# Kernel optimization log

Measured on AMD Instinct MI355X. Metric: run time of the kernel, lower is better.

The kernel has to match this reference:

```python
import jax, jax.numpy as jnp
import numpy as np

N = 50000      # nodes
E = 800000     # edges (avg degree 16)
IN, HID, OUT = 256, 128, 64
K, ALPHA = 4, 0.0  # APPNPConv(k=4, alpha=0.0)


def setup_inputs() -> dict:
    key = jax.random.key(0)
    ks = jax.random.split(key, 5)
    features = jax.random.normal(ks[0], (N, IN), jnp.float32)
    src = jax.random.randint(ks[1], (E,), 0, N, jnp.int32)
    dst = jax.random.randint(ks[2], (E,), 0, N, jnp.int32)
    W1 = jax.random.normal(ks[3], (IN, HID), jnp.float32) / np.float32(np.sqrt(IN))
    b1 = jnp.zeros((HID,), jnp.float32)
    W3 = jax.random.normal(ks[4], (HID, OUT), jnp.float32) / np.float32(np.sqrt(HID))
    b3 = jnp.zeros((OUT,), jnp.float32)
    return dict(features=features, src=src, dst=dst, W1=W1, b1=b1, W3=W3, b3=b3)


def _sym_norms(src, dst, n):
    # D_out^{-1/2} for source side, D_in^{-1/2} for destination side (DGL norm='both')
    ones = jnp.ones((src.shape[0],), jnp.float32)
    deg_out = jax.ops.segment_sum(ones, src, num_segments=n)
    deg_in = jax.ops.segment_sum(ones, dst, num_segments=n)
    return jnp.clip(deg_out, 1.0) ** -0.5, jnp.clip(deg_in, 1.0) ** -0.5


def _prop(x, src, dst, norm_src, norm_dst):
    # x: [N, D]. Symmetric-normalized SpMM: D_in^{-1/2} A D_out^{-1/2} x
    msg = (x * norm_src[:, None])[src]                       # [E, D] gather
    agg = jax.ops.segment_sum(msg, dst, num_segments=x.shape[0])  # [N, D] scatter-add
    return agg * norm_dst[:, None]


def reference(features, src, dst, W1, b1, W3, b3):
    ns, nd = _sym_norms(src, dst, N)
    # GraphConv 1 (weight-first since in_dim > hidden_dim; math identical either way)
    h = _prop(features @ W1, src, dst, ns, nd) + b1
    # dropout is identity in eval mode (training=False)
    # APPNPConv: k=4 power-iteration steps with teleport alpha=0.0
    h0 = h
    for _ in range(K):
        h = (1.0 - ALPHA) * _prop(h, src, dst, ns, nd) + ALPHA * h0
    # GraphConv 3
    out = _prop(h @ W3, src, dst, ns, nd) + b3
    return out
```

## Files before the change

### kernel.cpp

```cpp
#include <hip/hip_runtime.h>
#include <math.h>

#define N_NODES 50000
#define N_EDGES 800000
#define DIN 256
#define DHID 128
#define DOUT 64
#define CSTRIDE 64
#define ZROW N_NODES
#define HBLOCKS 256
#define HCHUNK (N_EDGES / HBLOCKS)
#define HWORDS (N_NODES / 4)
#define SLICE ((size_t)(N_NODES + 1) * 16)
#define NGROUPS (N_NODES / 4)
#define P2BLOCKS 196

#define SB_SENT 3125
#define SB_HS (SB_SENT + HBLOCKS)
#define SB_HD (SB_HS + HBLOCKS)
#define SB_TOT (SB_HD + 66)

__global__ void k_setup(const int* __restrict__ src, const int* __restrict__ dst,
                        unsigned int* __restrict__ pS, unsigned int* __restrict__ pD,
                        unsigned int* __restrict__ csr32,
                        const float* __restrict__ W1, const float* __restrict__ b1,
                        const float* __restrict__ W3,
                        float* __restrict__ W13, float* __restrict__ bb,
                        float* __restrict__ Y0, float* __restrict__ Y1) {
    __shared__ unsigned int h[HWORDS];
    int bx = blockIdx.x, t = threadIdx.x;
    if (bx < SB_SENT) {
        unsigned int v = (unsigned int)ZROW | ((unsigned int)ZROW << 16);
        uint2 o; o.x = v; o.y = v;
        ((uint2*)csr32)[bx * 256 + t] = o;
        return;
    }
    if (bx < SB_HD) {
        const int* idx = (bx < SB_HS) ? src : dst;
        unsigned int* outp = (bx < SB_HS) ? pS : pD;
        int hb = bx - ((bx < SB_HS) ? SB_SENT : SB_HS);
        for (int w = t; w < HWORDS; w += 256) h[w] = 0u;
        __syncthreads();
        int base = hb * HCHUNK;
        for (int i = t; i < HCHUNK; i += 256) {
            int s = idx[base + i];
            atomicAdd(&h[s >> 2], 1u << ((s & 3) << 3));
        }
        __syncthreads();
        outp += (size_t)hb * HWORDS;
        for (int w = t; w < HWORDS; w += 256) outp[w] = h[w];
        return;
    }
    int vb = bx - SB_HD;
    if (vb == 65) {
        if (t < 64) {
            int qq = t >> 4, c2 = t & 15;
            Y0[(size_t)qq * SLICE + ((size_t)ZROW << 4) + c2] = 0.f;
            Y1[(size_t)qq * SLICE + ((size_t)ZROW << 4) + c2] = 0.f;
        }
        return;
    }
    if (vb == 64) {
        if (t < DOUT) {
            float s = 0.f;
            for (int k = 0; k < DHID; ++k) s += b1[k] * W3[k * DOUT + t];
            bb[t] = s;
        }
        return;
    }
    int idx2 = vb * 256 + t;
    int i = idx2 >> 6, j = idx2 & 63;
    float s = 0.f;
    for (int k = 0; k < DHID; ++k) s += W1[i * DHID + k] * W3[k * DOUT + j];
    W13[idx2] = s;
}

__global__ void k_hpre(const unsigned int* __restrict__ pS,
                       const unsigned int* __restrict__ pD,
                       unsigned int* __restrict__ prefix,
                       int* __restrict__ deg_in,
                       float* __restrict__ ns, float* __restrict__ nd,
                       float* __restrict__ cc, int* __restrict__ dparts) {
    __shared__ unsigned int sdw[64][4];
    __shared__ unsigned int sow[64][4];
    __shared__ int lh[65];
    int t = threadIdx.x;
    if (t < 65) lh[t] = 0;
    int col = t >> 2, sub = t & 3;
    int wid = blockIdx.x * 64 + col;
    bool act = wid < HWORDS;
    unsigned int ps = 0, pd = 0;
    if (act) {
        int b0 = sub << 6;
#pragma unroll 4
        for (int b = b0; b < b0 + 64; ++b) {
            ps += pS[(size_t)b * HWORDS + wid];
            pd += pD[(size_t)b * HWORDS + wid];
        }
    }
    sdw[col][sub] = pd;
    sow[col][sub] = ps;
    __syncthreads();
    if (act) {
        unsigned int base = 0;
        for (int k = 0; k < sub; ++k) base += sdw[col][k];
        int b0 = sub << 6;
        unsigned int run = base;
        for (int b = b0; b < b0 + 64; ++b) {
            unsigned int w = pD[(size_t)b * HWORDS + wid];
            prefix[(size_t)b * HWORDS + wid] = run;
            run += w;
        }
        if (sub == 0) {
            unsigned int totd = sdw[col][0] + sdw[col][1] + sdw[col][2] + sdw[col][3];
            unsigned int toto = sow[col][0] + sow[col][1] + sow[col][2] + sow[col][3];
            unsigned int di[4] = {totd & 0xffu, (totd >> 8) & 0xffu,
                                  (totd >> 16) & 0xffu, totd >> 24};
            unsigned int dov[4] = {toto & 0xffu, (toto >> 8) & 0xffu,
                                   (toto >> 16) & 0xffu, toto >> 24};
            int4 dd; dd.x = (int)di[0]; dd.y = (int)di[1]; dd.z = (int)di[2]; dd.w = (int)di[3];
            *(int4*)(deg_in + (wid << 2)) = dd;
            float4 vns, vnd, vcc;
            float* pns = &vns.x; float* pnd = &vnd.x; float* pcc = &vcc.x;
#pragma unroll
            for (int q = 0; q < 4; ++q) {
                int bin = (int)di[q]; if (bin > 64) bin = 64;
                atomicAdd(&lh[bin], 1);
                unsigned int a = dov[q] < 1u ? 1u : dov[q];
                unsigned int b = di[q] < 1u ? 1u : di[q];
                float fa = 1.0f / sqrtf((float)a);
                float fb = 1.0f / sqrtf((float)b);
                pns[q] = fa; pnd[q] = fb; pcc[q] = fa * fb;
            }
            *(float4*)(ns + (wid << 2)) = vns;
            *(float4*)(nd + (wid << 2)) = vnd;
            *(float4*)(cc + (wid << 2)) = vcc;
        }
    }
    __syncthreads();
    if (t < 65) dparts[blockIdx.x * 65 + t] = lh[t];
}

__global__ void k_dscan(const int* __restrict__ dparts, int* __restrict__ offs) {
    __shared__ int colsum[65], binbase[65];
    int t = threadIdx.x;
    if (t < 65) {
        int s = 0;
        for (int b = 0; b < P2BLOCKS; ++b) s += dparts[b * 65 + t];
        colsum[t] = s;
    }
    __syncthreads();
    if (t == 0) {
        int run = 0;
        for (int k = 64; k >= 0; --k) { binbase[k] = run; run += colsum[k]; }
    }
    __syncthreads();
    if (t < 65) {
        int run = binbase[t];
        for (int b = 0; b < P2BLOCKS; ++b) { offs[b * 65 + t] = run; run += dparts[b * 65 + t]; }
    }
}

__global__ void k_dscatter(const int* __restrict__ deg_in, const int* __restrict__ offs,
                           const float* __restrict__ cc, const float* __restrict__ ns,
                           const float* __restrict__ nd,
                           int* __restrict__ perm, int* __restrict__ inv,
                           int* __restrict__ degP, float* __restrict__ ccP,
                           float* __restrict__ nsP, float* __restrict__ ndP) {
    __shared__ int off[65];
    int t = threadIdx.x;
    if (t < 65) off[t] = offs[blockIdx.x * 65 + t];
    __syncthreads();
    int wid = blockIdx.x * 64 + t;
    if (t < 64 && wid < HWORDS) {
        int4 d4 = *(const int4*)(deg_in + (wid << 2));
        int dd[4] = {d4.x, d4.y, d4.z, d4.w};
#pragma unroll
        for (int k = 0; k < 4; ++k) {
            int node = (wid << 2) + k;
            int bin = dd[k] > 64 ? 64 : dd[k];
            int slot = atomicAdd(&off[bin], 1);
            perm[slot] = node; inv[node] = slot;
            degP[slot] = dd[k];
            ccP[slot] = cc[node]; nsP[slot] = ns[node]; ndP[slot] = nd[node];
        }
    }
}

__global__ void k_fill(const int* __restrict__ src, const int* __restrict__ dst,
                       const unsigned int* __restrict__ prefix,
                       const int* __restrict__ inv,
                       unsigned short* __restrict__ csr) {
    __shared__ unsigned int h[HWORDS];
    int t = threadIdx.x;
    const unsigned int* prow = prefix + (size_t)blockIdx.x * HWORDS;
    for (int w = t; w < HWORDS; w += 256) h[w] = prow[w];
    __syncthreads();
    int base = blockIdx.x * HCHUNK;
    for (int i = t; i < HCHUNK; i += 256) {
        int s = src[base + i], d = dst[base + i];
        int sh = (d & 3) << 3;
        unsigned int old = atomicAdd(&h[d >> 2], 1u << sh);
        int slot = (int)((old >> sh) & 0xffu);
        csr[((size_t)inv[d] << 6) + slot] = (unsigned short)inv[s];
    }
}

__global__ void k_gemm(const float* __restrict__ X, const float* __restrict__ W13,
                       const float* __restrict__ ns, const int* __restrict__ inv,
                       float* __restrict__ Y) {
    __shared__ float As[16][68];
    __shared__ float Bs[16][64];
    int tid = threadIdx.x;
    int tx = tid & 15, ty = tid >> 4;
    int row0 = blockIdx.x * 64;
    float acc[4][4];
#pragma unroll
    for (int i = 0; i < 4; ++i)
#pragma unroll
        for (int j = 0; j < 4; ++j) acc[i][j] = 0.f;

    int lr = tid >> 2;
    int lk = (tid & 3) << 2;
    int arow = row0 + lr;
    if (arow > N_NODES - 1) arow = N_NODES - 1;

    for (int k0 = 0; k0 < DIN; k0 += 16) {
        float4 a = *(const float4*)(X + (size_t)arow * DIN + k0 + lk);
        As[lk + 0][lr] = a.x; As[lk + 1][lr] = a.y;
        As[lk + 2][lr] = a.z; As[lk + 3][lr] = a.w;
        float4 b = *(const float4*)(W13 + (size_t)(k0 + (tid >> 4)) * DOUT + ((tid & 15) << 2));
        *(float4*)&Bs[tid >> 4][(tid & 15) << 2] = b;
        __syncthreads();
#pragma unroll
        for (int k = 0; k < 16; ++k) {
            float4 av = *(const float4*)&As[k][ty << 2];
            float4 bv = *(const float4*)&Bs[k][tx << 2];
            float ar[4] = {av.x, av.y, av.z, av.w};
            float br[4] = {bv.x, bv.y, bv.z, bv.w};
#pragma unroll
            for (int i = 0; i < 4; ++i)
#pragma unroll
                for (int j = 0; j < 4; ++j) acc[i][j] += ar[i] * br[j];
        }
        __syncthreads();
    }
    int qq = tx >> 2;
    int co = (tx & 3) << 2;
#pragma unroll
    for (int i = 0; i < 4; ++i) {
        int row = row0 + (ty << 2) + i;
        if (row < N_NODES) {
            float nsr = ns[row];
            int prow = inv[row];
            float4 o;
            o.x = acc[i][0] * nsr; o.y = acc[i][1] * nsr;
            o.z = acc[i][2] * nsr; o.w = acc[i][3] * nsr;
            *(float4*)(Y + (size_t)qq * SLICE + ((size_t)prow << 4) + co) = o;
        }
    }
}


template <int MODE>
__launch_bounds__(256, 8)
__global__ void k_spmm(const float* __restrict__ xs, float* __restrict__ ys,
                       const unsigned short* __restrict__ csr,
                       const int* __restrict__ degP,
                       const float* __restrict__ ccP, const float* __restrict__ nsP,
                       const float* __restrict__ ndP,
                       const float* __restrict__ bb, const float* __restrict__ b3,
                       const int* __restrict__ perm) {
    __shared__ unsigned short rows[4][256];
    int wid  = threadIdx.x >> 6;
    int lane = threadIdx.x & 63;
    int q    = (blockIdx.x & 7) >> 1;
    int half = blockIdx.x & 1;
    int g    = (blockIdx.x >> 3) * 8 + wid * 2 + half;
    if (g >= NGROUPS) return;
    int node0 = g << 2;

    int nn = lane >> 4, sl = lane & 15;
    const uint2* crow = (const uint2*)(csr + ((size_t)(node0 + nn) << 6)) + sl;
    uint2 rv = *crow;
    unsigned short* bp = &rows[wid][(sl << 4) + nn];
    bp[0]  = (unsigned short)(rv.x & 0xffffu);
    bp[4]  = (unsigned short)(rv.x >> 16);
    bp[8]  = (unsigned short)(rv.y & 0xffffu);
    bp[12] = (unsigned short)(rv.y >> 16);

    int n0u = __builtin_amdgcn_readfirstlane(node0);
    int m = (degP[n0u] + 7) & ~7;

    int n = lane >> 4, e = (lane >> 2) & 3, c4 = lane & 3;
    const unsigned short* rd = &rows[wid][(e << 2) + n];
    const float* xq = xs + (size_t)q * SLICE + (c4 << 2);

    float ax = 0.f, ay = 0.f, az = 0.f, aw = 0.f;
#define LDV(T) const float4 v##T = *(const float4*)(xq + ((size_t)rd[16 * (T)] << 4))
#define ACCV(T) ax += v##T.x; ay += v##T.y; az += v##T.z; aw += v##T.w
    if (m <= 8) {
        LDV(0); LDV(1);
        ACCV(0); ACCV(1);
    } else if (m <= 16) {
        LDV(0); LDV(1); LDV(2); LDV(3);
        ACCV(0); ACCV(1); ACCV(2); ACCV(3);
    } else if (m <= 24) {
        LDV(0); LDV(1); LDV(2); LDV(3); LDV(4); LDV(5);
        ACCV(0); ACCV(1); ACCV(2); ACCV(3); ACCV(4); ACCV(5);
    } else if (m <= 32) {
        LDV(0); LDV(1); LDV(2); LDV(3); LDV(4); LDV(5); LDV(6); LDV(7);
        ACCV(0); ACCV(1); ACCV(2); ACCV(3); ACCV(4); ACCV(5); ACCV(6); ACCV(7);
    } else {
        for (int j2 = 0; j2 < m; j2 += 8) {
            int o = j2 << 2;
            const float4 a = *(const float4*)(xq + ((size_t)rd[o] << 4));
            const float4 b = *(const float4*)(xq + ((size_t)rd[o + 16] << 4));
            ax += a.x; ay += a.y; az += a.z; aw += a.w;
            ax += b.x; ay += b.y; az += b.z; aw += b.w;
        }
    }
#undef LDV
#undef ACCV
    ax += __shfl_xor(ax, 4);  ay += __shfl_xor(ay, 4);
    az += __shfl_xor(az, 4);  aw += __shfl_xor(aw, 4);
    ax += __shfl_xor(ax, 8);  ay += __shfl_xor(ay, 8);
    az += __shfl_xor(az, 8);  aw += __shfl_xor(aw, 8);

    int nodeL = node0 + n;
    int colq  = (q << 4) + (c4 << 2);
    float4 r;
    if (MODE == 0) {
        float cv = ccP[nodeL], nv = nsP[nodeL];
        float4 bv = *(const float4*)(bb + colq);
        r.x = cv * ax + nv * bv.x; r.y = cv * ay + nv * bv.y;
        r.z = cv * az + nv * bv.z; r.w = cv * aw + nv * bv.w;
    } else if (MODE == 1) {
        float cv = ccP[nodeL];
        r.x = cv * ax; r.y = cv * ay; r.z = cv * az; r.w = cv * aw;
    } else {
        float dv = ndP[nodeL];
        float4 bv = *(const float4*)(b3 + colq);
        r.x = dv * ax + bv.x; r.y = dv * ay + bv.y;
        r.z = dv * az + bv.z; r.w = dv * aw + bv.w;
    }
    if (e == 0) {
        if (MODE == 2) {
            int orow = perm[nodeL];
            *(float4*)(ys + ((size_t)orow << 6) + colq) = r;
        } else {
            *(float4*)(ys + (size_t)q * SLICE + ((size_t)nodeL << 4) + (c4 << 2)) = r;
        }
    }
}


extern "C" void kernel_launch(void* const* d_in, const int* in_sizes, int n_in,
                              void* d_out, int out_size, void* d_ws, size_t ws_size,
                              hipStream_t stream) {
    const float* X   = (const float*)d_in[0];
    const int*   src = (const int*)d_in[1];
    const int*   dst = (const int*)d_in[2];
    const float* W1  = (const float*)d_in[3];
    const float* b1  = (const float*)d_in[4];
    const float* W3  = (const float*)d_in[5];
    const float* b3  = (const float*)d_in[6];
    float* out = (float*)d_out;

    char* ws = (char*)d_ws;
    size_t off = 0;
    auto alloc = [&](size_t bytes) -> void* {
        void* p = ws + off;
        off = (off + bytes + 255) & ~(size_t)255;
        return p;
    };
    unsigned int*   pS     = (unsigned int*)alloc((size_t)HBLOCKS * HWORDS * 4);
    unsigned int*   pD     = (unsigned int*)alloc((size_t)HBLOCKS * HWORDS * 4);
    unsigned int*   pref   = (unsigned int*)alloc((size_t)HBLOCKS * HWORDS * 4);
    float*          Y0     = (float*)alloc(SLICE * 4 * 4);
    float*          Y1     = (float*)alloc(SLICE * 4 * 4);
    unsigned short* csr    = (unsigned short*)alloc((size_t)N_NODES * CSTRIDE * 2);
    int*            deg_in = (int*)alloc((size_t)N_NODES * 4);
    float*          ns     = (float*)alloc((size_t)N_NODES * 4);
    float*          nd     = (float*)alloc((size_t)N_NODES * 4);
    float*          cc     = (float*)alloc((size_t)N_NODES * 4);
    int*            perm   = (int*)alloc((size_t)N_NODES * 4);
    int*            inv    = (int*)alloc((size_t)N_NODES * 4);
    int*            degP   = (int*)alloc((size_t)N_NODES * 4);
    float*          ccP    = (float*)alloc((size_t)N_NODES * 4);
    float*          nsP    = (float*)alloc((size_t)N_NODES * 4);
    float*          ndP    = (float*)alloc((size_t)N_NODES * 4);
    int*            dparts = (int*)alloc((size_t)P2BLOCKS * 65 * 4);
    int*            offs   = (int*)alloc((size_t)P2BLOCKS * 65 * 4);
    float*          W13    = (float*)alloc((size_t)DIN * DOUT * 4);
    float*          bb     = (float*)alloc(DOUT * 4);

    const int sblk = 1563 * 8;

    k_setup<<<SB_TOT, 256, 0, stream>>>(src, dst, pS, pD, (unsigned int*)csr,
                                        W1, b1, W3, W13, bb, Y0, Y1);
    k_hpre<<<P2BLOCKS, 256, 0, stream>>>(pS, pD, pref, deg_in, ns, nd, cc, dparts);
    k_dscan<<<1, 128, 0, stream>>>(dparts, offs);
    k_dscatter<<<P2BLOCKS, 128, 0, stream>>>(deg_in, offs, cc, ns, nd,
                                             perm, inv, degP, ccP, nsP, ndP);
    k_fill<<<HBLOCKS, 256, 0, stream>>>(src, dst, pref, inv, csr);

    k_gemm<<<(N_NODES + 63) / 64, 256, 0, stream>>>(X, W13, ns, inv, Y0);

    k_spmm<0><<<sblk, 256, 0, stream>>>(Y0, Y1, csr, degP, ccP, nsP, ndP, bb, b3, perm);
    k_spmm<1><<<sblk, 256, 0, stream>>>(Y1, Y0, csr, degP, ccP, nsP, ndP, bb, b3, perm);
    k_spmm<1><<<sblk, 256, 0, stream>>>(Y0, Y1, csr, degP, ccP, nsP, ndP, bb, b3, perm);
    k_spmm<1><<<sblk, 256, 0, stream>>>(Y1, Y0, csr, degP, ccP, nsP, ndP, bb, b3, perm);
    k_spmm<1><<<sblk, 256, 0, stream>>>(Y0, Y1, csr, degP, ccP, nsP, ndP, bb, b3, perm);
    k_spmm<2><<<sblk, 256, 0, stream>>>(Y1, out, csr, degP, ccP, nsP, ndP, bb, b3, perm);
}
```

Before: 304.3 us.

## Replace histogram/prefix CSR build with global atomics and drop degree permutation

Replaces the multi-kernel packed-histogram, prefix-scan and degree-sorted permutation pipeline with global atomic degree counting and atomic slot assignment into a fixed-stride CSR. The GEMM, normalization prep and CSR fill are fused into one multi-role kernel. The SpMM switches from a four-way column-sliced layout with warp shuffles to a row-major 64-wide layout where each lane covers 16 columns, using a per-group max degree instead of sorted degrees. This removes several launches and large partial-histogram traffic, but loses degree-sorted load balancing, adds contended global atomics, and makes the CSR slot order nondeterministic.

```diff
diff --git a/kernel.cpp b/kernel.cpp
--- a/kernel.cpp
+++ b/kernel.cpp
@@ -8,26 +8,23 @@
 #define DOUT 64
 #define CSTRIDE 64
 #define ZROW N_NODES
-#define HBLOCKS 256
-#define HCHUNK (N_EDGES / HBLOCKS)
-#define HWORDS (N_NODES / 4)
-#define SLICE ((size_t)(N_NODES + 1) * 16)
-#define NGROUPS (N_NODES / 4)
-#define P2BLOCKS 196
+#define NG4 12500
+#define NPAD 50176
+
+#define DEGBLK 256
+#define DCHUNK (N_EDGES / DEGBLK)
 
 #define SB_SENT 3125
-#define SB_HS (SB_SENT + HBLOCKS)
-#define SB_HD (SB_HS + HBLOCKS)
-#define SB_TOT (SB_HD + 66)
+#define SB_DEG  (SB_SENT + DEGBLK)
+#define SB_TOT  (SB_DEG + 66)
 
 __global__ void k_setup(const int* __restrict__ src, const int* __restrict__ dst,
-                        unsigned int* __restrict__ pS, unsigned int* __restrict__ pD,
+                        unsigned int* __restrict__ degS, unsigned int* __restrict__ degD,
                         unsigned int* __restrict__ csr32,
                         const float* __restrict__ W1, const float* __restrict__ b1,
                         const float* __restrict__ W3,
                         float* __restrict__ W13, float* __restrict__ bb,
                         float* __restrict__ Y0, float* __restrict__ Y1) {
-    __shared__ unsigned int h[HWORDS];
     int bx = blockIdx.x, t = threadIdx.x;
     if (bx < SB_SENT) {
         unsigned int v = (unsigned int)ZROW | ((unsigned int)ZROW << 16);
@@ -35,29 +32,18 @@
         ((uint2*)csr32)[bx * 256 + t] = o;
         return;
     }
-    if (bx < SB_HD) {
-        const int* idx = (bx < SB_HS) ? src : dst;
-        unsigned int* outp = (bx < SB_HS) ? pS : pD;
-        int hb = bx - ((bx < SB_HS) ? SB_SENT : SB_HS);
-        for (int w = t; w < HWORDS; w += 256) h[w] = 0u;
-        __syncthreads();
-        int base = hb * HCHUNK;
-        for (int i = t; i < HCHUNK; i += 256) {
-            int s = idx[base + i];
-            atomicAdd(&h[s >> 2], 1u << ((s & 3) << 3));
-        }
-        __syncthreads();
-        outp += (size_t)hb * HWORDS;
-        for (int w = t; w < HWORDS; w += 256) outp[w] = h[w];
+    if (bx < SB_DEG) {
+        int base = (bx - SB_SENT) * DCHUNK;
+        for (int i = t; i < DCHUNK; i += 256) {
+            atomicAdd(&degS[src[base + i]], 1u);
+            atomicAdd(&degD[dst[base + i]], 1u);
+        }
         return;
     }
-    int vb = bx - SB_HD;
+    int vb = bx - SB_DEG;
     if (vb == 65) {
-        if (t < 64) {
-            int qq = t >> 4, c2 = t & 15;
-            Y0[(size_t)qq * SLICE + ((size_t)ZROW << 4) + c2] = 0.f;
-            Y1[(size_t)qq * SLICE + ((size_t)ZROW << 4) + c2] = 0.f;
-        }
+        if (t < 64) Y0[(size_t)ZROW * 64 + t] = 0.f;
+        else if (t < 128) Y1[(size_t)ZROW * 64 + (t - 64)] = 0.f;
         return;
     }
     if (vb == 64) {
@@ -75,188 +61,103 @@
     W13[idx2] = s;
 }
 
-__global__ void k_hpre(const unsigned int* __restrict__ pS,
-                       const unsigned int* __restrict__ pD,
-                       unsigned int* __restrict__ prefix,
-                       int* __restrict__ deg_in,
-                       float* __restrict__ ns, float* __restrict__ nd,
-                       float* __restrict__ cc, int* __restrict__ dparts) {
-    __shared__ unsigned int sdw[64][4];
-    __shared__ unsigned int sow[64][4];
-    __shared__ int lh[65];
-    int t = threadIdx.x;
-    if (t < 65) lh[t] = 0;
-    int col = t >> 2, sub = t & 3;
-    int wid = blockIdx.x * 64 + col;
-    bool act = wid < HWORDS;
-    unsigned int ps = 0, pd = 0;
-    if (act) {
-        int b0 = sub << 6;
-#pragma unroll 4
-        for (int b = b0; b < b0 + 64; ++b) {
-            ps += pS[(size_t)b * HWORDS + wid];
-            pd += pD[(size_t)b * HWORDS + wid];
-        }
-    }
-    sdw[col][sub] = pd;
-    sow[col][sub] = ps;
-    __syncthreads();
-    if (act) {
-        unsigned int base = 0;
-        for (int k = 0; k < sub; ++k) base += sdw[col][k];
-        int b0 = sub << 6;
-        unsigned int run = base;
-        for (int b = b0; b < b0 + 64; ++b) {
-            unsigned int w = pD[(size_t)b * HWORDS + wid];
-            prefix[(size_t)b * HWORDS + wid] = run;
-            run += w;
-        }
-        if (sub == 0) {
-            unsigned int totd = sdw[col][0] + sdw[col][1] + sdw[col][2] + sdw[col][3];
-            unsigned int toto = sow[col][0] + sow[col][1] + sow[col][2] + sow[col][3];
-            unsigned int di[4] = {totd & 0xffu, (totd >> 8) & 0xffu,
-                                  (totd >> 16) & 0xffu, totd >> 24};
-            unsigned int dov[4] = {toto & 0xffu, (toto >> 8) & 0xffu,
-                                   (toto >> 16) & 0xffu, toto >> 24};
-            int4 dd; dd.x = (int)di[0]; dd.y = (int)di[1]; dd.z = (int)di[2]; dd.w = (int)di[3];
-            *(int4*)(deg_in + (wid << 2)) = dd;
-            float4 vns, vnd, vcc;
-            float* pns = &vns.x; float* pnd = &vnd.x; float* pcc = &vcc.x;
-#pragma unroll
-            for (int q = 0; q < 4; ++q) {
-                int bin = (int)di[q]; if (bin > 64) bin = 64;
-                atomicAdd(&lh[bin], 1);
-                unsigned int a = dov[q] < 1u ? 1u : dov[q];
-                unsigned int b = di[q] < 1u ? 1u : di[q];
-                float fa = 1.0f / sqrtf((float)a);
-                float fb = 1.0f / sqrtf((float)b);
-                pns[q] = fa; pnd[q] = fb; pcc[q] = fa * fb;
+#define MB_GEMM 782
+#define MB_PREP 196
+#define MB_FILL 256
+#define MB_TOT (MB_GEMM + MB_PREP + MB_FILL)
+
+__global__ void k_mid(const float* __restrict__ X, const float* __restrict__ W13,
+                      const unsigned int* __restrict__ degS,
+                      const unsigned int* __restrict__ degD,
+                      const int* __restrict__ src, const int* __restrict__ dst,
+                      unsigned int* __restrict__ cnt, unsigned short* __restrict__ csr,
+                      float* __restrict__ ns, float* __restrict__ nd,
+                      float* __restrict__ cc, int* __restrict__ mG,
+                      float* __restrict__ Y) {
+    int bx = blockIdx.x, tid = threadIdx.x;
+    if (bx < MB_GEMM) {
+        __shared__ float As[16][68];
+        __shared__ float Bs[16][64];
+        int tx = tid & 15, ty = tid >> 4;
+        int row0 = bx * 64;
+        float acc[4][4];
+#pragma unroll
+        for (int i = 0; i < 4; ++i)
+#pragma unroll
+            for (int j = 0; j < 4; ++j) acc[i][j] = 0.f;
+        int lr = tid >> 2;
+        int lk = (tid & 3) << 2;
+        int arow = row0 + lr;
+        if (arow > N_NODES - 1) arow = N_NODES - 1;
+        for (int k0 = 0; k0 < DIN; k0 += 16) {
+            float4 a = *(const float4*)(X + (size_t)arow * DIN + k0 + lk);
+            As[lk + 0][lr] = a.x; As[lk + 1][lr] = a.y;
+            As[lk + 2][lr] = a.z; As[lk + 3][lr] = a.w;
+            float4 b = *(const float4*)(W13 + (size_t)(k0 + (tid >> 4)) * DOUT + ((tid & 15) << 2));
+            *(float4*)&Bs[tid >> 4][(tid & 15) << 2] = b;
+            __syncthreads();
+#pragma unroll
+            for (int k = 0; k < 16; ++k) {
+                float4 av = *(const float4*)&As[k][ty << 2];
+                float4 bv = *(const float4*)&Bs[k][tx << 2];
+                float ar[4] = {av.x, av.y, av.z, av.w};
+                float br[4] = {bv.x, bv.y, bv.z, bv.w};
+#pragma unroll
+                for (int i = 0; i < 4; ++i)
+#pragma unroll
+                    for (int j = 0; j < 4; ++j) acc[i][j] += ar[i] * br[j];
             }
-            *(float4*)(ns + (wid << 2)) = vns;
-            *(float4*)(nd + (wid << 2)) = vnd;
-            *(float4*)(cc + (wid << 2)) = vcc;
-        }
-    }
-    __syncthreads();
-    if (t < 65) dparts[blockIdx.x * 65 + t] = lh[t];
-}
-
-__global__ void k_dscan(const int* __restrict__ dparts, int* __restrict__ offs) {
-    __shared__ int colsum[65], binbase[65];
-    int t = threadIdx.x;
-    if (t < 65) {
-        int s = 0;
-        for (int b = 0; b < P2BLOCKS; ++b) s += dparts[b * 65 + t];
-        colsum[t] = s;
-    }
-    __syncthreads();
-    if (t == 0) {
-        int run = 0;
-        for (int k = 64; k >= 0; --k) { binbase[k] = run; run += colsum[k]; }
-    }
-    __syncthreads();
-    if (t < 65) {
-        int run = binbase[t];
-        for (int b = 0; b < P2BLOCKS; ++b) { offs[b * 65 + t] = run; run += dparts[b * 65 + t]; }
-    }
-}
-
-__global__ void k_dscatter(const int* __restrict__ deg_in, const int* __restrict__ offs,
-                           const float* __restrict__ cc, const float* __restrict__ ns,
-                           const float* __restrict__ nd,
-                           int* __restrict__ perm, int* __restrict__ inv,
-                           int* __restrict__ degP, float* __restrict__ ccP,
-                           float* __restrict__ nsP, float* __restrict__ ndP) {
-    __shared__ int off[65];
-    int t = threadIdx.x;
-    if (t < 65) off[t] = offs[blockIdx.x * 65 + t];
-    __syncthreads();
-    int wid = blockIdx.x * 64 + t;
-    if (t < 64 && wid < HWORDS) {
-        int4 d4 = *(const int4*)(deg_in + (wid << 2));
-        int dd[4] = {d4.x, d4.y, d4.z, d4.w};
-#pragma unroll
-        for (int k = 0; k < 4; ++k) {
-            int node = (wid << 2) + k;
-            int bin = dd[k] > 64 ? 64 : dd[k];
-            int slot = atomicAdd(&off[bin], 1);
-            perm[slot] = node; inv[node] = slot;
-            degP[slot] = dd[k];
-            ccP[slot] = cc[node]; nsP[slot] = ns[node]; ndP[slot] = nd[node];
-        }
-    }
-}
-
-__global__ void k_fill(const int* __restrict__ src, const int* __restrict__ dst,
-                       const unsigned int* __restrict__ prefix,
-                       const int* __restrict__ inv,
-                       unsigned short* __restrict__ csr) {
-    __shared__ unsigned int h[HWORDS];
-    int t = threadIdx.x;
-    const unsigned int* prow = prefix + (size_t)blockIdx.x * HWORDS;
-    for (int w = t; w < HWORDS; w += 256) h[w] = prow[w];
-    __syncthreads();
-    int base = blockIdx.x * HCHUNK;
-    for (int i = t; i < HCHUNK; i += 256) {
-        int s = src[base + i], d = dst[base + i];
-        int sh = (d & 3) << 3;
-        unsigned int old = atomicAdd(&h[d >> 2], 1u << sh);
-        int slot = (int)((old >> sh) & 0xffu);
-        csr[((size_t)inv[d] << 6) + slot] = (unsigned short)inv[s];
-    }
-}
-
-__global__ void k_gemm(const float* __restrict__ X, const float* __restrict__ W13,
-                       const float* __restrict__ ns, const int* __restrict__ inv,
-                       float* __restrict__ Y) {
-    __shared__ float As[16][68];
-    __shared__ float Bs[16][64];
-    int tid = threadIdx.x;
-    int tx = tid & 15, ty = tid >> 4;
-    int row0 = blockIdx.x * 64;
-    float acc[4][4];
-#pragma unroll
-    for (int i = 0; i < 4; ++i)
-#pragma unroll
-        for (int j = 0; j < 4; ++j) acc[i][j] = 0.f;
-
-    int lr = tid >> 2;
-    int lk = (tid & 3) << 2;
-    int arow = row0 + lr;
-    if (arow > N_NODES - 1) arow = N_NODES - 1;
-
-    for (int k0 = 0; k0 < DIN; k0 += 16) {
-        float4 a = *(const float4*)(X + (size_t)arow * DIN + k0 + lk);
-        As[lk + 0][lr] = a.x; As[lk + 1][lr] = a.y;
-        As[lk + 2][lr] = a.z; As[lk + 3][lr] = a.w;
-        float4 b = *(const float4*)(W13 + (size_t)(k0 + (tid >> 4)) * DOUT + ((tid & 15) << 2));
-        *(float4*)&Bs[tid >> 4][(tid & 15) << 2] = b;
-        __syncthreads();
-#pragma unroll
-        for (int k = 0; k < 16; ++k) {
-            float4 av = *(const float4*)&As[k][ty << 2];
-            float4 bv = *(const float4*)&Bs[k][tx << 2];
-            float ar[4] = {av.x, av.y, av.z, av.w};
-            float br[4] = {bv.x, bv.y, bv.z, bv.w};
-#pragma unroll
-            for (int i = 0; i < 4; ++i)
-#pragma unroll
-                for (int j = 0; j < 4; ++j) acc[i][j] += ar[i] * br[j];
-        }
-        __syncthreads();
-    }
-    int qq = tx >> 2;
-    int co = (tx & 3) << 2;
-#pragma unroll
-    for (int i = 0; i < 4; ++i) {
-        int row = row0 + (ty << 2) + i;
-        if (row < N_NODES) {
-            float nsr = ns[row];
-            int prow = inv[row];
-            float4 o;
-            o.x = acc[i][0] * nsr; o.y = acc[i][1] * nsr;
-            o.z = acc[i][2] * nsr; o.w = acc[i][3] * nsr;
-            *(float4*)(Y + (size_t)qq * SLICE + ((size_t)prow << 4) + co) = o;
+            __syncthreads();
+        }
+        int qq = tx >> 2;
+        int co = (tx & 3) << 2;
+#pragma unroll
+        for (int i = 0; i < 4; ++i) {
+            int row = row0 + (ty << 2) + i;
+            if (row < N_NODES) {
+                unsigned int dsv = degS[row];
+                float nsr = rsqrtf((float)(dsv ? dsv : 1u));
+                float4 o;
+                o.x = acc[i][0] * nsr; o.y = acc[i][1] * nsr;
+                o.z = acc[i][2] * nsr; o.w = acc[i][3] * nsr;
+                *(float4*)(Y + (size_t)row * 64 + (qq << 4) + co) = o;
+            }
+        }
+    } else if (bx < MB_GEMM + MB_PREP) {
+        if (tid < 64) {
+            int wid = (bx - MB_GEMM) * 64 + tid;
+            if (wid < NG4) {
+                uint4 s4 = *(const uint4*)(degS + (wid << 2));
+                uint4 d4 = *(const uint4*)(degD + (wid << 2));
+                unsigned int dsv[4] = {s4.x, s4.y, s4.z, s4.w};
+                unsigned int ddv[4] = {d4.x, d4.y, d4.z, d4.w};
+                float fns[4], fnd[4], fcc[4];
+                unsigned int mx = 0;
+#pragma unroll
+                for (int q = 0; q < 4; ++q) {
+                    if (ddv[q] > mx) mx = ddv[q];
+                    unsigned int a = dsv[q] ? dsv[q] : 1u;
+                    unsigned int b = ddv[q] ? ddv[q] : 1u;
+                    float fa = rsqrtf((float)a);
+                    float fb = rsqrtf((float)b);
+                    fns[q] = fa; fnd[q] = fb; fcc[q] = fa * fb;
+                }
+                float4 vns = {fns[0], fns[1], fns[2], fns[3]};
+                float4 vnd = {fnd[0], fnd[1], fnd[2], fnd[3]};
+                float4 vcc = {fcc[0], fcc[1], fcc[2], fcc[3]};
+                *(float4*)(ns + (wid << 2)) = vns;
+                *(float4*)(nd + (wid << 2)) = vnd;
+                *(float4*)(cc + (wid << 2)) = vcc;
+                int m = ((int)mx + 7) & ~7;
+                mG[wid] = m > 64 ? 64 : m;
+            }
+        }
+    } else {
+        int base = (bx - MB_GEMM - MB_PREP) * DCHUNK;
+        for (int i = tid; i < DCHUNK; i += 256) {
+            int s = src[base + i], d = dst[base + i];
+            unsigned int slot = atomicAdd(&cnt[d], 1u);
+            if (slot < 64u) csr[((size_t)d << 6) + slot] = (unsigned short)s;
         }
     }
 }
@@ -266,92 +167,95 @@
 __launch_bounds__(256, 8)
 __global__ void k_spmm(const float* __restrict__ xs, float* __restrict__ ys,
                        const unsigned short* __restrict__ csr,
-                       const int* __restrict__ degP,
-                       const float* __restrict__ ccP, const float* __restrict__ nsP,
-                       const float* __restrict__ ndP,
-                       const float* __restrict__ bb, const float* __restrict__ b3,
-                       const int* __restrict__ perm) {
+                       const int* __restrict__ mG,
+                       const float* __restrict__ cc, const float* __restrict__ ns,
+                       const float* __restrict__ nd,
+                       const float* __restrict__ bb, const float* __restrict__ b3) {
     __shared__ unsigned short rows[4][256];
-    int wid  = threadIdx.x >> 6;
-    int lane = threadIdx.x & 63;
-    int q    = (blockIdx.x & 7) >> 1;
-    int half = blockIdx.x & 1;
-    int g    = (blockIdx.x >> 3) * 8 + wid * 2 + half;
-    if (g >= NGROUPS) return;
+    int wid = threadIdx.x >> 6, lane = threadIdx.x & 63;
+    int g = blockIdx.x * 4 + wid;
     int node0 = g << 2;
-
-    int nn = lane >> 4, sl = lane & 15;
-    const uint2* crow = (const uint2*)(csr + ((size_t)(node0 + nn) << 6)) + sl;
-    uint2 rv = *crow;
-    unsigned short* bp = &rows[wid][(sl << 4) + nn];
+    int n = lane >> 4, sl = lane & 15;
+    uint2 rv = *((const uint2*)(csr + ((size_t)(node0 + n) << 6)) + sl);
+    unsigned short* bp = &rows[wid][(sl << 4) + n];
     bp[0]  = (unsigned short)(rv.x & 0xffffu);
     bp[4]  = (unsigned short)(rv.x >> 16);
     bp[8]  = (unsigned short)(rv.y & 0xffffu);
     bp[12] = (unsigned short)(rv.y >> 16);
 
-    int n0u = __builtin_amdgcn_readfirstlane(node0);
-    int m = (degP[n0u] + 7) & ~7;
-
-    int n = lane >> 4, e = (lane >> 2) & 3, c4 = lane & 3;
-    const unsigned short* rd = &rows[wid][(e << 2) + n];
-    const float* xq = xs + (size_t)q * SLICE + (c4 << 2);
-
+    int m = __builtin_amdgcn_readfirstlane(mG[g]);
+
+    int c16 = lane & 15;
+    const unsigned short* rd = &rows[wid][n];
+    const float* xq = xs + (c16 << 2);
     float ax = 0.f, ay = 0.f, az = 0.f, aw = 0.f;
-#define LDV(T) const float4 v##T = *(const float4*)(xq + ((size_t)rd[16 * (T)] << 4))
-#define ACCV(T) ax += v##T.x; ay += v##T.y; az += v##T.z; aw += v##T.w
+#define LD(T) const float4 v##T = *(const float4*)(xq + ((size_t)rd[(T) << 2] << 6))
+#define AC(T) ax += v##T.x; ay += v##T.y; az += v##T.z; aw += v##T.w
     if (m <= 8) {
-        LDV(0); LDV(1);
-        ACCV(0); ACCV(1);
+        LD(0); LD(1); LD(2); LD(3); LD(4); LD(5); LD(6); LD(7);
+        AC(0); AC(1); AC(2); AC(3); AC(4); AC(5); AC(6); AC(7);
     } else if (m <= 16) {
-        LDV(0); LDV(1); LDV(2); LDV(3);
-        ACCV(0); ACCV(1); ACCV(2); ACCV(3);
+        LD(0); LD(1); LD(2); LD(3); LD(4); LD(5); LD(6); LD(7);
+        AC(0); LD(8);  AC(1); LD(9);  AC(2); LD(10); AC(3); LD(11);
+        AC(4); LD(12); AC(5); LD(13); AC(6); LD(14); AC(7); LD(15);
+        AC(8); AC(9); AC(10); AC(11); AC(12); AC(13); AC(14); AC(15);
     } else if (m <= 24) {
-        LDV(0); LDV(1); LDV(2); LDV(3); LDV(4); LDV(5);
-        ACCV(0); ACCV(1); ACCV(2); ACCV(3); ACCV(4); ACCV(5);
+        LD(0); LD(1); LD(2); LD(3); LD(4); LD(5); LD(6); LD(7);
+        AC(0);  LD(8);  AC(1);  LD(9);  AC(2);  LD(10); AC(3);  LD(11);
+        AC(4);  LD(12); AC(5);  LD(13); AC(6);  LD(14); AC(7);  LD(15);
+        AC(8);  LD(16); AC(9);  LD(17); AC(10); LD(18); AC(11); LD(19);
+        AC(12); LD(20); AC(13); LD(21); AC(14); LD(22); AC(15); LD(23);
+        AC(16); AC(17); AC(18); AC(19); AC(20); AC(21); AC(22); AC(23);
     } else if (m <= 32) {
-        LDV(0); LDV(1); LDV(2); LDV(3); LDV(4); LDV(5); LDV(6); LDV(7);
-        ACCV(0); ACCV(1); ACCV(2); ACCV(3); ACCV(4); ACCV(5); ACCV(6); ACCV(7);
+        LD(0); LD(1); LD(2); LD(3); LD(4); LD(5); LD(6); LD(7);
+        AC(0);  LD(8);  AC(1);  LD(9);  AC(2);  LD(10); AC(3);  LD(11);
+        AC(4);  LD(12); AC(5);  LD(13); AC(6);  LD(14); AC(7);  LD(15);
+        AC(8);  LD(16); AC(9);  LD(17); AC(10); LD(18); AC(11); LD(19);
+        AC(12); LD(20); AC(13); LD(21); AC(14); LD(22); AC(15); LD(23);
+        AC(16); LD(24); AC(17); LD(25); AC(18); LD(26); AC(19); LD(27);
+        AC(20); LD(28); AC(21); LD(29); AC(22); LD(30); AC(23); LD(31);
+        AC(24); AC(25); AC(26); AC(27); AC(28); AC(29); AC(30); AC(31);
     } else {
-        for (int j2 = 0; j2 < m; j2 += 8) {
-            int o = j2 << 2;
-            const float4 a = *(const float4*)(xq + ((size_t)rd[o] << 4));
-            const float4 b = *(const float4*)(xq + ((size_t)rd[o + 16] << 4));
-            ax += a.x; ay += a.y; az += a.z; aw += a.w;
-            ax += b.x; ay += b.y; az += b.z; aw += b.w;
-        }
-    }
-#undef LDV
-#undef ACCV
-    ax += __shfl_xor(ax, 4);  ay += __shfl_xor(ay, 4);
-    az += __shfl_xor(az, 4);  aw += __shfl_xor(aw, 4);
-    ax += __shfl_xor(ax, 8);  ay += __shfl_xor(ay, 8);
-    az += __shfl_xor(az, 8);  aw += __shfl_xor(aw, 8);
-
-    int nodeL = node0 + n;
-    int colq  = (q << 4) + (c4 << 2);
+        for (int T = 0; T < m; T += 8) {
+            int o = T << 2;
+            const float4 w0 = *(const float4*)(xq + ((size_t)rd[o]      << 6));
+            const float4 w1 = *(const float4*)(xq + ((size_t)rd[o + 4]  << 6));
+            const float4 w2 = *(const float4*)(xq + ((size_t)rd[o + 8]  << 6));
+            const float4 w3 = *(const float4*)(xq + ((size_t)rd[o + 12] << 6));
+            const float4 w4 = *(const float4*)(xq + ((size_t)rd[o + 16] << 6));
+            const float4 w5 = *(const float4*)(xq + ((size_t)rd[o + 20] << 6));
+            const float4 w6 = *(const float4*)(xq + ((size_t)rd[o + 24] << 6));
+            const float4 w7 = *(const float4*)(xq + ((size_t)rd[o + 28] << 6));
+            ax += w0.x; ay += w0.y; az += w0.z; aw += w0.w;
+            ax += w1.x; ay += w1.y; az += w1.z; aw += w1.w;
+            ax += w2.x; ay += w2.y; az += w2.z; aw += w2.w;
+            ax += w3.x; ay += w3.y; az += w3.z; aw += w3.w;
+            ax += w4.x; ay += w4.y; az += w4.z; aw += w4.w;
+            ax += w5.x; ay += w5.y; az += w5.z; aw += w5.w;
+            ax += w6.x; ay += w6.y; az += w6.z; aw += w6.w;
+            ax += w7.x; ay += w7.y; az += w7.z; aw += w7.w;
+        }
+    }
+#undef LD
+#undef AC
+    int node = node0 + n;
+    int col = c16 << 2;
     float4 r;
     if (MODE == 0) {
-        float cv = ccP[nodeL], nv = nsP[nodeL];
-        float4 bv = *(const float4*)(bb + colq);
+        float cv = cc[node], nv = ns[node];
+        float4 bv = *(const float4*)(bb + col);
         r.x = cv * ax + nv * bv.x; r.y = cv * ay + nv * bv.y;
         r.z = cv * az + nv * bv.z; r.w = cv * aw + nv * bv.w;
     } else if (MODE == 1) {
-        float cv = ccP[nodeL];
+        float cv = cc[node];
         r.x = cv * ax; r.y = cv * ay; r.z = cv * az; r.w = cv * aw;
     } else {
-        float dv = ndP[nodeL];
-        float4 bv = *(const float4*)(b3 + colq);
+        float dv = nd[node];
+        float4 bv = *(const float4*)(b3 + col);
         r.x = dv * ax + bv.x; r.y = dv * ay + bv.y;
         r.z = dv * az + bv.z; r.w = dv * aw + bv.w;
     }
-    if (e == 0) {
-        if (MODE == 2) {
-            int orow = perm[nodeL];
-            *(float4*)(ys + ((size_t)orow << 6) + colq) = r;
-        } else {
-            *(float4*)(ys + (size_t)q * SLICE + ((size_t)nodeL << 4) + (c4 << 2)) = r;
-        }
-    }
+    *(float4*)(ys + ((size_t)node << 6) + col) = r;
 }
 
 
@@ -374,43 +278,32 @@
         off = (off + bytes + 255) & ~(size_t)255;
         return p;
     };
-    unsigned int*   pS     = (unsigned int*)alloc((size_t)HBLOCKS * HWORDS * 4);
-    unsigned int*   pD     = (unsigned int*)alloc((size_t)HBLOCKS * HWORDS * 4);
-    unsigned int*   pref   = (unsigned int*)alloc((size_t)HBLOCKS * HWORDS * 4);
-    float*          Y0     = (float*)alloc(SLICE * 4 * 4);
-    float*          Y1     = (float*)alloc(SLICE * 4 * 4);
-    unsigned short* csr    = (unsigned short*)alloc((size_t)N_NODES * CSTRIDE * 2);
-    int*            deg_in = (int*)alloc((size_t)N_NODES * 4);
-    float*          ns     = (float*)alloc((size_t)N_NODES * 4);
-    float*          nd     = (float*)alloc((size_t)N_NODES * 4);
-    float*          cc     = (float*)alloc((size_t)N_NODES * 4);
-    int*            perm   = (int*)alloc((size_t)N_NODES * 4);
-    int*            inv    = (int*)alloc((size_t)N_NODES * 4);
-    int*            degP   = (int*)alloc((size_t)N_NODES * 4);
-    float*          ccP    = (float*)alloc((size_t)N_NODES * 4);
-    float*          nsP    = (float*)alloc((size_t)N_NODES * 4);
-    float*          ndP    = (float*)alloc((size_t)N_NODES * 4);
-    int*            dparts = (int*)alloc((size_t)P2BLOCKS * 65 * 4);
-    int*            offs   = (int*)alloc((size_t)P2BLOCKS * 65 * 4);
-    float*          W13    = (float*)alloc((size_t)DIN * DOUT * 4);
-    float*          bb     = (float*)alloc(DOUT * 4);
-
-    const int sblk = 1563 * 8;
-
-    k_setup<<<SB_TOT, 256, 0, stream>>>(src, dst, pS, pD, (unsigned int*)csr,
+    unsigned int*   zreg = (unsigned int*)alloc((size_t)3 * NPAD * 4);
+    unsigned int*   degS = zreg;
+    unsigned int*   degD = zreg + NPAD;
+    unsigned int*   cnt  = zreg + 2 * NPAD;
+    float*          Y0   = (float*)alloc((size_t)(N_NODES + 1) * 64 * 4);
+    float*          Y1   = (float*)alloc((size_t)(N_NODES + 1) * 64 * 4);
+    unsigned short* csr  = (unsigned short*)alloc((size_t)N_NODES * CSTRIDE * 2);
+    float*          ns   = (float*)alloc((size_t)N_NODES * 4);
+    float*          nd   = (float*)alloc((size_t)N_NODES * 4);
+    float*          cc   = (float*)alloc((size_t)N_NODES * 4);
+    int*            mG   = (int*)alloc((size_t)NG4 * 4);
+    float*          W13  = (float*)alloc((size_t)DIN * DOUT * 4);
+    float*          bb   = (float*)alloc(DOUT * 4);
+
+    hipMemsetAsync(zreg, 0, (size_t)3 * NPAD * 4, stream);
+
+    k_setup<<<SB_TOT, 256, 0, stream>>>(src, dst, degS, degD, (unsigned int*)csr,
                                         W1, b1, W3, W13, bb, Y0, Y1);
-    k_hpre<<<P2BLOCKS, 256, 0, stream>>>(pS, pD, pref, deg_in, ns, nd, cc, dparts);
-    k_dscan<<<1, 128, 0, stream>>>(dparts, offs);
-    k_dscatter<<<P2BLOCKS, 128, 0, stream>>>(deg_in, offs, cc, ns, nd,
-                                             perm, inv, degP, ccP, nsP, ndP);
-    k_fill<<<HBLOCKS, 256, 0, stream>>>(src, dst, pref, inv, csr);
-
-    k_gemm<<<(N_NODES + 63) / 64, 256, 0, stream>>>(X, W13, ns, inv, Y0);
-
-    k_spmm<0><<<sblk, 256, 0, stream>>>(Y0, Y1, csr, degP, ccP, nsP, ndP, bb, b3, perm);
-    k_spmm<1><<<sblk, 256, 0, stream>>>(Y1, Y0, csr, degP, ccP, nsP, ndP, bb, b3, perm);
-    k_spmm<1><<<sblk, 256, 0, stream>>>(Y0, Y1, csr, degP, ccP, nsP, ndP, bb, b3, perm);
-    k_spmm<1><<<sblk, 256, 0, stream>>>(Y1, Y0, csr, degP, ccP, nsP, ndP, bb, b3, perm);
-    k_spmm<1><<<sblk, 256, 0, stream>>>(Y0, Y1, csr, degP, ccP, nsP, ndP, bb, b3, perm);
-    k_spmm<2><<<sblk, 256, 0, stream>>>(Y1, out, csr, degP, ccP, nsP, ndP, bb, b3, perm);
+
+    k_mid<<<MB_TOT, 256, 0, stream>>>(X, W13, degS, degD, src, dst, cnt, csr,
+                                      ns, nd, cc, mG, Y0);
+
+    k_spmm<0><<<3125, 256, 0, stream>>>(Y0, Y1, csr, mG, cc, ns, nd, bb, b3);
+    k_spmm<1><<<3125, 256, 0, stream>>>(Y1, Y0, csr, mG, cc, ns, nd, bb, b3);
+    k_spmm<1><<<3125, 256, 0, stream>>>(Y0, Y1, csr, mG, cc, ns, nd, bb, b3);
+    k_spmm<1><<<3125, 256, 0, stream>>>(Y1, Y0, csr, mG, cc, ns, nd, bb, b3);
+    k_spmm<1><<<3125, 256, 0, stream>>>(Y0, Y1, csr, mG, cc, ns, nd, bb, b3);
+    k_spmm<2><<<3125, 256, 0, stream>>>(Y1, out, csr, mG, cc, ns, nd, bb, b3);
 }
```

Result: slower. 362.1 us (+19.0%).
